# Kernel tuning notes

Measured on AMD Instinct MI355X. Metric: run time of the kernel, lower is better.

## Reference

```python
import jax, jax.numpy as jnp
import numpy as np

K = 8           # neighbor_num
H = 8           # n_heads
DH = 64         # dim_single_head


def setup_inputs() -> dict:
    key = jax.random.key(0)
    ks = jax.random.split(key, 6)
    B, N, D = 2, 8192, 256
    inner = H * DH  # 512
    x = jax.random.normal(ks[0], (B, N, D), jnp.float32)
    center_pos3d = jax.random.normal(ks[1], (B, N, 3), jnp.float32)
    Wq = jax.random.normal(ks[2], (D, inner), jnp.float32) * 0.02
    Wkv = jax.random.normal(ks[3], (D, 2 * inner), jnp.float32) * 0.02
    Wout = jax.random.normal(ks[4], (inner, D), jnp.float32) * 0.02
    bout = jnp.zeros((D,), jnp.float32)
    return {"x": x, "center_pos3d": center_pos3d, "Wq": Wq, "Wkv": Wkv,
            "Wout": Wout, "bout": bout}


def _knn_idx(pos, k):
    # pos: [B,N,3] -> indices of k nearest neighbors per point, [B,N,k]
    sq = jnp.sum(pos * pos, axis=-1)                      # [B,N]
    d2 = sq[:, :, None] + sq[:, None, :] - 2.0 * jnp.einsum('bnc,bmc->bnm', pos, pos)
    _, idx = jax.lax.top_k(-d2, k)                        # smallest distances
    return idx


def reference(x, center_pos3d, Wq, Wkv, Wout, bout):
    B, N, D = x.shape
    inner = H * DH
    scale = DH ** -0.5

    idx = _knn_idx(center_pos3d, K)                       # [B,N,K] int32
    # grouping_operation: gather neighbor features -> [B,N,K,D]
    knn_x = jax.vmap(lambda xb, ib: xb[ib])(x, idx)

    q = (x @ Wq).reshape(B, N, H, DH)                     # [B,N,H,DH]
    kv = knn_x @ Wkv                                      # [B,N,K,2*inner]
    k_, v_ = jnp.split(kv, 2, axis=-1)
    k_ = k_.reshape(B, N, K, H, DH)
    v_ = v_.reshape(B, N, K, H, DH)

    dots = jnp.einsum('bnhd,bnkhd->bnhk', q, k_) * scale  # [B,N,H,K]
    attn = jax.nn.softmax(dots, axis=-1)
    out = jnp.einsum('bnhk,bnkhd->bnhd', attn, v_)        # [B,N,H,DH]
    out = out.reshape(B, N, inner)
    return out @ Wout + bout                              # dropout p=0 -> identity
```

## Files before the change

### kernel.cpp

```cpp
#include <hip/hip_runtime.h>
#include <hip/hip_bf16.h>

#define N_PTS 8192
#define KNN 8

typedef __attribute__((ext_vector_type(8))) short short8;
typedef __attribute__((ext_vector_type(4))) float float4v;

static __device__ __forceinline__ short f2bf(float f) {
    unsigned u = __float_as_uint(f);
    unsigned r = (u + 0x7FFFu + ((u >> 16) & 1u)) >> 16;
    return (short)r;
}
static __device__ __forceinline__ float bf2f(short s) {
    return __uint_as_float(((unsigned)(unsigned short)s) << 16);
}

__global__ __launch_bounds__(256) void knn_partial(const float* __restrict__ pos,
                                                   unsigned long long* __restrict__ partial)
{
    __shared__ float sx[512], sy[512], sz[512];
    __shared__ unsigned long long buf[256][17];

    const int tid = threadIdx.x;
    const int p   = blockIdx.x & 15;
    const int qg  = blockIdx.x >> 4;
    const int batch = qg >> 5;
    const int q_in_b = (qg & 31) * 256 + tid;
    const float* bpos = pos + (long)batch * N_PTS * 3;

    if (tid < 128) {
        const float* src = bpos + (p * 512 + tid * 4) * 3;
        const float4 f0 = *(const float4*)(src);
        const float4 f1 = *(const float4*)(src + 4);
        const float4 f2 = *(const float4*)(src + 8);
        const int c0 = tid * 4;
        *(float4*)&sx[c0] = make_float4(f0.x, f0.w, f1.z, f2.y);
        *(float4*)&sy[c0] = make_float4(f0.y, f1.x, f1.w, f2.z);
        *(float4*)&sz[c0] = make_float4(f0.z, f1.y, f2.x, f2.w);
    }
    __syncthreads();

    const float qx = bpos[q_in_b * 3 + 0];
    const float qy = bpos[q_in_b * 3 + 1];
    const float qz = bpos[q_in_b * 3 + 2];

    const float4* vx = (const float4*)sx;
    const float4* vy = (const float4*)sy;
    const float4* vz = (const float4*)sz;

    float bmin[32];
#pragma unroll
    for (int j = 0; j < 32; ++j) bmin[j] = 3.0e38f;

    for (int base = 0; base < 128; base += 8) {
#pragma unroll
        for (int g = 0; g < 8; ++g) {
            const float4 cx = vx[base + g];
            const float4 cy = vy[base + g];
            const float4 cz = vz[base + g];
            { const float dx = cx.x - qx, dy = cy.x - qy, dz = cz.x - qz;
              bmin[g*4+0] = fminf(bmin[g*4+0], fmaf(dx, dx, fmaf(dy, dy, dz*dz))); }
            { const float dx = cx.y - qx, dy = cy.y - qy, dz = cz.y - qz;
              bmin[g*4+1] = fminf(bmin[g*4+1], fmaf(dx, dx, fmaf(dy, dy, dz*dz))); }
            { const float dx = cx.z - qx, dy = cy.z - qy, dz = cz.z - qz;
              bmin[g*4+2] = fminf(bmin[g*4+2], fmaf(dx, dx, fmaf(dy, dy, dz*dz))); }
            { const float dx = cx.w - qx, dy = cy.w - qy, dz = cz.w - qz;
              bmin[g*4+3] = fminf(bmin[g*4+3], fmaf(dx, dx, fmaf(dy, dy, dz*dz))); }
        }
    }

    float t8[8];
#pragma unroll
    for (int j = 0; j < 8; ++j) t8[j] = 3.0e38f;
#pragma unroll
    for (int i = 0; i < 32; ++i) {
        float x = bmin[i];
#pragma unroll
        for (int j = 0; j < 8; ++j) {
            const float lo = fminf(t8[j], x);
            const float hi = fmaxf(t8[j], x);
            t8[j] = lo; x = hi;
        }
    }
    const float t = t8[7];

    int cnt = 0;
    for (int base = 0; base < 128; ++base) {
        const float4 cx = vx[base];
        const float4 cy = vy[base];
        const float4 cz = vz[base];
#pragma unroll
        for (int j = 0; j < 4; ++j) {
            const float ccx = j == 0 ? cx.x : j == 1 ? cx.y : j == 2 ? cx.z : cx.w;
            const float ccy = j == 0 ? cy.x : j == 1 ? cy.y : j == 2 ? cy.z : cy.w;
            const float ccz = j == 0 ? cz.x : j == 1 ? cz.y : j == 2 ? cz.z : cz.w;
            const float dx = ccx - qx, dy = ccy - qy, dz = ccz - qz;
            const float d2 = fmaf(dx, dx, fmaf(dy, dy, dz * dz));
            if (d2 <= t) {
                buf[tid][cnt < 16 ? cnt : 16] =
                    ((unsigned long long)__float_as_uint(d2) << 32)
                    | (unsigned)(p * 512 + base * 4 + j);
                ++cnt;
            }
        }
    }

    unsigned long long best[8];
#pragma unroll
    for (int j = 0; j < 8; ++j) best[j] = ~0ULL;

    if (cnt <= 16) {
        for (int u = 0; u < cnt; ++u) {
            unsigned long long x = buf[tid][u];
#pragma unroll
            for (int j = 0; j < 8; ++j) {
                const unsigned long long lo = x < best[j] ? x : best[j];
                const unsigned long long hi = x < best[j] ? best[j] : x;
                best[j] = lo; x = hi;
            }
        }
    } else {
        for (int i = 0; i < 512; ++i) {
            const float dx = sx[i] - qx, dy = sy[i] - qy, dz = sz[i] - qz;
            const float d2 = fmaf(dx, dx, fmaf(dy, dy, dz * dz));
            unsigned long long x =
                ((unsigned long long)__float_as_uint(d2) << 32)
                | (unsigned)(p * 512 + i);
            if (x < best[7]) {
#pragma unroll
                for (int j = 0; j < 8; ++j) {
                    const unsigned long long lo = x < best[j] ? x : best[j];
                    const unsigned long long hi = x < best[j] ? best[j] : x;
                    best[j] = lo; x = hi;
                }
            }
        }
    }

    const long qglob = (long)batch * N_PTS + q_in_b;
#pragma unroll
    for (int j = 0; j < 8; ++j)
        partial[(long)(p * 8 + j) * 16384 + qglob] = best[j];
}

__global__ __launch_bounds__(256) void knn_merge(const unsigned long long* __restrict__ partial,
                                                 int* __restrict__ idxo)
{
    const int q = blockIdx.x * 256 + threadIdx.x;
    unsigned long long best[8];
#pragma unroll
    for (int j = 0; j < 8; ++j) best[j] = ~0ULL;
    for (int s = 0; s < 128; ++s) {
        unsigned long long x = partial[(long)s * 16384 + q];
        if (x < best[7]) {
#pragma unroll
            for (int j = 0; j < 8; ++j) {
                const unsigned long long lo = x < best[j] ? x : best[j];
                const unsigned long long hi = x < best[j] ? best[j] : x;
                best[j] = lo; x = hi;
            }
        }
    }
#pragma unroll
    for (int j = 0; j < 8; ++j)
        idxo[(long)q * 8 + j] = (int)(best[j] & 0xFFFFFFFFu);
}

template<int ABF16, int OUTBF16>
__global__ __launch_bounds__(256) void gemm_bf16(const void* __restrict__ A_,
                                                 const float* __restrict__ B,
                                                 const float* __restrict__ bias,
                                                 void* __restrict__ C_,
                                                 int N, int Kd, int lda)
{
    __shared__ short As[4][128][8];
    __shared__ short Bs[4][128][8];

    const int tid  = threadIdx.x;
    const int lane = tid & 63;
    const int wv   = tid >> 6;
    const int quad = lane >> 4;
    const int l15  = lane & 15;
    const int m0 = blockIdx.y * 128;
    const int n0 = blockIdx.x * 128;
    const int mh = (wv & 1) * 64, nh = (wv >> 1) * 64;

    const int sm  = tid >> 1;
    const int skh = (tid & 1) * 16;
    const int sn  = tid & 127;
    const int skb = (tid >> 7) * 16;

    float4v acc[4][4];
#pragma unroll
    for (int i = 0; i < 4; ++i)
#pragma unroll
        for (int j = 0; j < 4; ++j) acc[i][j] = (float4v)(0.f);

    for (int k0 = 0; k0 < Kd; k0 += 32) {
        if (ABF16) {
            const short* Ab = (const short*)A_;
            const short8* src = (const short8*)(Ab + (long)(m0 + sm) * lda + k0 + skh);
            *(short8*)&As[skh >> 3][sm][0] = src[0];
            *(short8*)&As[(skh >> 3) + 1][sm][0] = src[1];
        } else {
            const float* Af = (const float*)A_;
            const float* ap = Af + (long)(m0 + sm) * lda + k0 + skh;
            const float4 a0 = *(const float4*)ap;
            const float4 a1 = *(const float4*)(ap + 4);
            const float4 a2 = *(const float4*)(ap + 8);
            const float4 a3 = *(const float4*)(ap + 12);
            short8 w0 = {f2bf(a0.x), f2bf(a0.y), f2bf(a0.z), f2bf(a0.w),
                         f2bf(a1.x), f2bf(a1.y), f2bf(a1.z), f2bf(a1.w)};
            short8 w1 = {f2bf(a2.x), f2bf(a2.y), f2bf(a2.z), f2bf(a2.w),
                         f2bf(a3.x), f2bf(a3.y), f2bf(a3.z), f2bf(a3.w)};
            *(short8*)&As[skh >> 3][sm][0] = w0;
            *(short8*)&As[(skh >> 3) + 1][sm][0] = w1;
        }
        {
            const float* bp = B + (long)(k0 + skb) * N + n0 + sn;
            short v[16];
#pragma unroll
            for (int kk = 0; kk < 16; ++kk)
                v[kk] = f2bf(bp[(long)kk * N]);
            short8 w0 = {v[0], v[1], v[2], v[3], v[4], v[5], v[6], v[7]};
            short8 w1 = {v[8], v[9], v[10], v[11], v[12], v[13], v[14], v[15]};
            *(short8*)&Bs[skb >> 3][sn][0] = w0;
            *(short8*)&Bs[(skb >> 3) + 1][sn][0] = w1;
        }
        __syncthreads();

        short8 af[4], bfv[4];
#pragma unroll
        for (int i = 0; i < 4; ++i)
            af[i] = *(const short8*)&As[quad][mh + i * 16 + l15][0];
#pragma unroll
        for (int j = 0; j < 4; ++j)
            bfv[j] = *(const short8*)&Bs[quad][nh + j * 16 + l15][0];
#pragma unroll
        for (int i = 0; i < 4; ++i)
#pragma unroll
            for (int j = 0; j < 4; ++j)
                acc[i][j] = __builtin_amdgcn_mfma_f32_16x16x32_bf16(af[i], bfv[j], acc[i][j], 0, 0, 0);
        __syncthreads();
    }

#pragma unroll
    for (int i = 0; i < 4; ++i)
#pragma unroll
        for (int j = 0; j < 4; ++j) {
            const int col = n0 + nh + j * 16 + l15;
            const float bb = (!OUTBF16 && bias) ? bias[col] : 0.f;
#pragma unroll
            for (int r = 0; r < 4; ++r) {
                const int row = m0 + mh + i * 16 + quad * 4 + r;
                if (OUTBF16) {
                    ((short*)C_)[(long)row * N + col] = f2bf(acc[i][j][r]);
                } else {
                    ((float*)C_)[(long)row * N + col] = acc[i][j][r] + bb;
                }
            }
        }
}

__global__ __launch_bounds__(256) void attn_kernel(const short* qall,
                                                   const short* __restrict__ kvall,
                                                   const int* __restrict__ idxp,
                                                   short* outp)
{
    __shared__ float attn_s[4][8][8];
    const int wave = threadIdx.x >> 6;
    const int lane = threadIdx.x & 63;
    const int g = blockIdx.x * 4 + wave;
    const int b = g >> 13;
    const int* myidx = idxp + (long)g * 8;

    {
        const int h = lane >> 3;
        const int k = lane & 7;
        const int j = myidx[k];
        const short8* qrow = (const short8*)(qall + (long)g * 512 + h * 64);
        const short8* krow = (const short8*)(kvall + ((long)(b * N_PTS + j)) * 1024 + h * 64);

        float dot = 0.f;
#pragma unroll
        for (int c = 0; c < 8; ++c) {
            const short8 qv = qrow[c];
            const short8 kv = krow[c];
#pragma unroll
            for (int e = 0; e < 8; ++e)
                dot = fmaf(bf2f(qv[e]), bf2f(kv[e]), dot);
        }
        dot *= 0.125f;

        float m = dot;
#pragma unroll
        for (int off = 1; off < 8; off <<= 1)
            m = fmaxf(m, __shfl_xor(m, off, 8));
        const float e = __expf(dot - m);
        float ssum = e;
#pragma unroll
        for (int off = 1; off < 8; off <<= 1)
            ssum += __shfl_xor(ssum, off, 8);
        attn_s[wave][h][k] = e / ssum;
    }
    __syncthreads();

    const int d8 = lane * 8;
    const int h2 = lane >> 3;
    float o[8] = {0.f, 0.f, 0.f, 0.f, 0.f, 0.f, 0.f, 0.f};
#pragma unroll
    for (int kk = 0; kk < 8; ++kk) {
        const int jj = myidx[kk];
        const float w = attn_s[wave][h2][kk];
        const short8 v = *(const short8*)(kvall + ((long)(b * N_PTS + jj)) * 1024 + 512 + d8);
#pragma unroll
        for (int e = 0; e < 8; ++e)
            o[e] = fmaf(w, bf2f(v[e]), o[e]);
    }
    short8 ov = {f2bf(o[0]), f2bf(o[1]), f2bf(o[2]), f2bf(o[3]),
                 f2bf(o[4]), f2bf(o[5]), f2bf(o[6]), f2bf(o[7])};
    *(short8*)(outp + (long)g * 512 + d8) = ov;
}

extern "C" void kernel_launch(void* const* d_in, const int* in_sizes, int n_in,
                              void* d_out, int out_size, void* d_ws, size_t ws_size,
                              hipStream_t stream)
{
    const float* x    = (const float*)d_in[0];
    const float* pos  = (const float*)d_in[1];
    const float* Wq   = (const float*)d_in[2];
    const float* Wkv  = (const float*)d_in[3];
    const float* Wout = (const float*)d_in[4];
    const float* bout = (const float*)d_in[5];
    float* out = (float*)d_out;

    int*   idxp = (int*)d_ws;
    short* qall = (short*)((char*)d_ws + (1 << 19));
    short* kvall = qall + (long)16384 * 512;
    unsigned long long* partial = (unsigned long long*)kvall;

    const int M = 16384;

    knn_partial<<<1024, 256, 0, stream>>>(pos, partial);
    knn_merge<<<64, 256, 0, stream>>>(partial, idxp);
    gemm_bf16<0, 1><<<dim3(512 / 128, M / 128), 256, 0, stream>>>(x, Wq, nullptr, qall, 512, 256, 256);
    gemm_bf16<0, 1><<<dim3(1024 / 128, M / 128), 256, 0, stream>>>(x, Wkv, nullptr, kvall, 1024, 256, 256);
    attn_kernel<<<M / 4, 256, 0, stream>>>(qall, kvall, idxp, qall);
    gemm_bf16<1, 0><<<dim3(256 / 128, M / 128), 256, 0, stream>>>(qall, Wout, bout, out, 256, 512, 512);
}
```

Measured before the change: 321.5 us.

## Use dot-product KNN with larger tiles and pre-converted bf16 GEMM operands

The KNN partial kernel now stores each candidate as a float4 holding xyz and half its squared norm. It screens candidates with a single 3-FMA dot-product score instead of a full distance, and processes 1024 candidates per block, which halves the partial slices and the merge work. A small epsilon widens the screening threshold, and exact distances are recomputed for the final ordering. The GEMMs now read x and transposed weights that separate conversion kernels have already turned into bf16, which removes per-tile fp32-to-bf16 conversion and the strided weight loads. This adds extra kernel launches and conversion passes on every call.

```diff
diff --git a/kernel.cpp b/kernel.cpp
--- a/kernel.cpp
+++ b/kernel.cpp
@@ -6,6 +6,7 @@
 
 typedef __attribute__((ext_vector_type(8))) short short8;
 typedef __attribute__((ext_vector_type(4))) float float4v;
+typedef unsigned long long u64;
 
 static __device__ __forceinline__ short f2bf(float f) {
     unsigned u = __float_as_uint(f);
@@ -17,27 +18,31 @@
 }
 
 __global__ __launch_bounds__(256) void knn_partial(const float* __restrict__ pos,
-                                                   unsigned long long* __restrict__ partial)
-{
-    __shared__ float sx[512], sy[512], sz[512];
-    __shared__ unsigned long long buf[256][17];
+                                                   u64* __restrict__ partial)
+{
+    __shared__ float4 sc[1024];
+    __shared__ u64 buf[256][17];
 
     const int tid = threadIdx.x;
-    const int p   = blockIdx.x & 15;
-    const int qg  = blockIdx.x >> 4;
+    const int p   = blockIdx.x & 7;
+    const int qg  = blockIdx.x >> 3;
     const int batch = qg >> 5;
     const int q_in_b = (qg & 31) * 256 + tid;
     const float* bpos = pos + (long)batch * N_PTS * 3;
 
-    if (tid < 128) {
-        const float* src = bpos + (p * 512 + tid * 4) * 3;
+    {
+        const float* src = bpos + (p * 1024 + tid * 4) * 3;
         const float4 f0 = *(const float4*)(src);
         const float4 f1 = *(const float4*)(src + 4);
         const float4 f2 = *(const float4*)(src + 8);
-        const int c0 = tid * 4;
-        *(float4*)&sx[c0] = make_float4(f0.x, f0.w, f1.z, f2.y);
-        *(float4*)&sy[c0] = make_float4(f0.y, f1.x, f1.w, f2.z);
-        *(float4*)&sz[c0] = make_float4(f0.z, f1.y, f2.x, f2.w);
+        sc[tid * 4 + 0] = make_float4(f0.x, f0.y, f0.z,
+            0.5f * fmaf(f0.x, f0.x, fmaf(f0.y, f0.y, f0.z * f0.z)));
+        sc[tid * 4 + 1] = make_float4(f0.w, f1.x, f1.y,
+            0.5f * fmaf(f0.w, f0.w, fmaf(f1.x, f1.x, f1.y * f1.y)));
+        sc[tid * 4 + 2] = make_float4(f1.z, f1.w, f2.x,
+            0.5f * fmaf(f1.z, f1.z, fmaf(f1.w, f1.w, f2.x * f2.x)));
+        sc[tid * 4 + 3] = make_float4(f2.y, f2.z, f2.w,
+            0.5f * fmaf(f2.y, f2.y, fmaf(f2.z, f2.z, f2.w * f2.w)));
     }
     __syncthreads();
 
@@ -45,28 +50,16 @@
     const float qy = bpos[q_in_b * 3 + 1];
     const float qz = bpos[q_in_b * 3 + 2];
 
-    const float4* vx = (const float4*)sx;
-    const float4* vy = (const float4*)sy;
-    const float4* vz = (const float4*)sz;
-
     float bmin[32];
 #pragma unroll
     for (int j = 0; j < 32; ++j) bmin[j] = 3.0e38f;
 
-    for (int base = 0; base < 128; base += 8) {
-#pragma unroll
-        for (int g = 0; g < 8; ++g) {
-            const float4 cx = vx[base + g];
-            const float4 cy = vy[base + g];
-            const float4 cz = vz[base + g];
-            { const float dx = cx.x - qx, dy = cy.x - qy, dz = cz.x - qz;
-              bmin[g*4+0] = fminf(bmin[g*4+0], fmaf(dx, dx, fmaf(dy, dy, dz*dz))); }
-            { const float dx = cx.y - qx, dy = cy.y - qy, dz = cz.y - qz;
-              bmin[g*4+1] = fminf(bmin[g*4+1], fmaf(dx, dx, fmaf(dy, dy, dz*dz))); }
-            { const float dx = cx.z - qx, dy = cy.z - qy, dz = cz.z - qz;
-              bmin[g*4+2] = fminf(bmin[g*4+2], fmaf(dx, dx, fmaf(dy, dy, dz*dz))); }
-            { const float dx = cx.w - qx, dy = cy.w - qy, dz = cz.w - qz;
-              bmin[g*4+3] = fminf(bmin[g*4+3], fmaf(dx, dx, fmaf(dy, dy, dz*dz))); }
+    for (int base = 0; base < 1024; base += 32) {
+#pragma unroll
+        for (int j = 0; j < 32; ++j) {
+            const float4 c = sc[base + j];
+            const float s = fmaf(-qx, c.x, fmaf(-qy, c.y, fmaf(-qz, c.z, c.w)));
+            bmin[j] = fminf(bmin[j], s);
         }
     }
 
@@ -83,55 +76,46 @@
             t8[j] = lo; x = hi;
         }
     }
-    const float t = t8[7];
+    const float t = t8[7] + 1e-4f;
 
     int cnt = 0;
-    for (int base = 0; base < 128; ++base) {
-        const float4 cx = vx[base];
-        const float4 cy = vy[base];
-        const float4 cz = vz[base];
-#pragma unroll
-        for (int j = 0; j < 4; ++j) {
-            const float ccx = j == 0 ? cx.x : j == 1 ? cx.y : j == 2 ? cx.z : cx.w;
-            const float ccy = j == 0 ? cy.x : j == 1 ? cy.y : j == 2 ? cy.z : cy.w;
-            const float ccz = j == 0 ? cz.x : j == 1 ? cz.y : j == 2 ? cz.z : cz.w;
-            const float dx = ccx - qx, dy = ccy - qy, dz = ccz - qz;
+    for (int i = 0; i < 1024; ++i) {
+        const float4 c = sc[i];
+        const float s = fmaf(-qx, c.x, fmaf(-qy, c.y, fmaf(-qz, c.z, c.w)));
+        if (s <= t) {
+            const float dx = c.x - qx, dy = c.y - qy, dz = c.z - qz;
             const float d2 = fmaf(dx, dx, fmaf(dy, dy, dz * dz));
-            if (d2 <= t) {
-                buf[tid][cnt < 16 ? cnt : 16] =
-                    ((unsigned long long)__float_as_uint(d2) << 32)
-                    | (unsigned)(p * 512 + base * 4 + j);
-                ++cnt;
-            }
-        }
-    }
-
-    unsigned long long best[8];
+            buf[tid][cnt < 16 ? cnt : 16] =
+                ((u64)__float_as_uint(d2) << 32) | (unsigned)(p * 1024 + i);
+            ++cnt;
+        }
+    }
+
+    u64 best[8];
 #pragma unroll
     for (int j = 0; j < 8; ++j) best[j] = ~0ULL;
 
     if (cnt <= 16) {
         for (int u = 0; u < cnt; ++u) {
-            unsigned long long x = buf[tid][u];
+            u64 x = buf[tid][u];
 #pragma unroll
             for (int j = 0; j < 8; ++j) {
-                const unsigned long long lo = x < best[j] ? x : best[j];
-                const unsigned long long hi = x < best[j] ? best[j] : x;
+                const u64 lo = x < best[j] ? x : best[j];
+                const u64 hi = x < best[j] ? best[j] : x;
                 best[j] = lo; x = hi;
             }
         }
     } else {
-        for (int i = 0; i < 512; ++i) {
-            const float dx = sx[i] - qx, dy = sy[i] - qy, dz = sz[i] - qz;
+        for (int i = 0; i < 1024; ++i) {
+            const float4 c = sc[i];
+            const float dx = c.x - qx, dy = c.y - qy, dz = c.z - qz;
             const float d2 = fmaf(dx, dx, fmaf(dy, dy, dz * dz));
-            unsigned long long x =
-                ((unsigned long long)__float_as_uint(d2) << 32)
-                | (unsigned)(p * 512 + i);
+            u64 x = ((u64)__float_as_uint(d2) << 32) | (unsigned)(p * 1024 + i);
             if (x < best[7]) {
 #pragma unroll
                 for (int j = 0; j < 8; ++j) {
-                    const unsigned long long lo = x < best[j] ? x : best[j];
-                    const unsigned long long hi = x < best[j] ? best[j] : x;
+                    const u64 lo = x < best[j] ? x : best[j];
+                    const u64 hi = x < best[j] ? best[j] : x;
                     best[j] = lo; x = hi;
                 }
             }
@@ -144,20 +128,20 @@
         partial[(long)(p * 8 + j) * 16384 + qglob] = best[j];
 }
 
-__global__ __launch_bounds__(256) void knn_merge(const unsigned long long* __restrict__ partial,
+__global__ __launch_bounds__(256) void knn_merge(const u64* __restrict__ partial,
                                                  int* __restrict__ idxo)
 {
     const int q = blockIdx.x * 256 + threadIdx.x;
-    unsigned long long best[8];
+    u64 best[8];
 #pragma unroll
     for (int j = 0; j < 8; ++j) best[j] = ~0ULL;
-    for (int s = 0; s < 128; ++s) {
-        unsigned long long x = partial[(long)s * 16384 + q];
+    for (int s = 0; s < 64; ++s) {
+        u64 x = partial[(long)s * 16384 + q];
         if (x < best[7]) {
 #pragma unroll
             for (int j = 0; j < 8; ++j) {
-                const unsigned long long lo = x < best[j] ? x : best[j];
-                const unsigned long long hi = x < best[j] ? best[j] : x;
+                const u64 lo = x < best[j] ? x : best[j];
+                const u64 hi = x < best[j] ? best[j] : x;
                 best[j] = lo; x = hi;
             }
         }
@@ -167,15 +151,37 @@
         idxo[(long)q * 8 + j] = (int)(best[j] & 0xFFFFFFFFu);
 }
 
-template<int ABF16, int OUTBF16>
-__global__ __launch_bounds__(256) void gemm_bf16(const void* __restrict__ A_,
-                                                 const float* __restrict__ B,
-                                                 const float* __restrict__ bias,
-                                                 void* __restrict__ C_,
-                                                 int N, int Kd, int lda)
-{
-    __shared__ short As[4][128][8];
-    __shared__ short Bs[4][128][8];
+__global__ __launch_bounds__(256) void conv_x(const float* __restrict__ x,
+                                              short* __restrict__ xb)
+{
+    const int i = blockIdx.x * 256 + threadIdx.x;
+    const float4 a = ((const float4*)x)[i * 2];
+    const float4 b = ((const float4*)x)[i * 2 + 1];
+    short8 w = {f2bf(a.x), f2bf(a.y), f2bf(a.z), f2bf(a.w),
+                f2bf(b.x), f2bf(b.y), f2bf(b.z), f2bf(b.w)};
+    ((short8*)xb)[i] = w;
+}
+
+__global__ __launch_bounds__(256) void conv_wt(const float* __restrict__ W,
+                                               short* __restrict__ Wt,
+                                               int kshift, int N)
+{
+    const int o = blockIdx.x * 256 + threadIdx.x;
+    const int K = 1 << kshift;
+    const int n = o >> kshift;
+    const int k = o & (K - 1);
+    Wt[o] = f2bf(W[(long)k * N + n]);
+}
+
+template<int OUTBF16>
+__global__ __launch_bounds__(256) void gemm_tt(const short* __restrict__ A,
+                                               const short* __restrict__ Bt,
+                                               const float* __restrict__ bias,
+                                               void* __restrict__ C_,
+                                               int N, int Kd)
+{
+    __shared__ short As[128][40];
+    __shared__ short Bs[128][40];
 
     const int tid  = threadIdx.x;
     const int lane = tid & 63;
@@ -186,10 +192,8 @@
     const int n0 = blockIdx.x * 128;
     const int mh = (wv & 1) * 64, nh = (wv >> 1) * 64;
 
-    const int sm  = tid >> 1;
-    const int skh = (tid & 1) * 16;
-    const int sn  = tid & 127;
-    const int skb = (tid >> 7) * 16;
+    const int srow  = tid >> 1;
+    const int shalf = (tid & 1) * 16;
 
     float4v acc[4][4];
 #pragma unroll
@@ -198,45 +202,21 @@
         for (int j = 0; j < 4; ++j) acc[i][j] = (float4v)(0.f);
 
     for (int k0 = 0; k0 < Kd; k0 += 32) {
-        if (ABF16) {
-            const short* Ab = (const short*)A_;
-            const short8* src = (const short8*)(Ab + (long)(m0 + sm) * lda + k0 + skh);
-            *(short8*)&As[skh >> 3][sm][0] = src[0];
-            *(short8*)&As[(skh >> 3) + 1][sm][0] = src[1];
-        } else {
-            const float* Af = (const float*)A_;
-            const float* ap = Af + (long)(m0 + sm) * lda + k0 + skh;
-            const float4 a0 = *(const float4*)ap;
-            const float4 a1 = *(const float4*)(ap + 4);
-            const float4 a2 = *(const float4*)(ap + 8);
-            const float4 a3 = *(const float4*)(ap + 12);
-            short8 w0 = {f2bf(a0.x), f2bf(a0.y), f2bf(a0.z), f2bf(a0.w),
-                         f2bf(a1.x), f2bf(a1.y), f2bf(a1.z), f2bf(a1.w)};
-            short8 w1 = {f2bf(a2.x), f2bf(a2.y), f2bf(a2.z), f2bf(a2.w),
-                         f2bf(a3.x), f2bf(a3.y), f2bf(a3.z), f2bf(a3.w)};
-            *(short8*)&As[skh >> 3][sm][0] = w0;
-            *(short8*)&As[(skh >> 3) + 1][sm][0] = w1;
-        }
-        {
-            const float* bp = B + (long)(k0 + skb) * N + n0 + sn;
-            short v[16];
-#pragma unroll
-            for (int kk = 0; kk < 16; ++kk)
-                v[kk] = f2bf(bp[(long)kk * N]);
-            short8 w0 = {v[0], v[1], v[2], v[3], v[4], v[5], v[6], v[7]};
-            short8 w1 = {v[8], v[9], v[10], v[11], v[12], v[13], v[14], v[15]};
-            *(short8*)&Bs[skb >> 3][sn][0] = w0;
-            *(short8*)&Bs[(skb >> 3) + 1][sn][0] = w1;
-        }
+        const short8* asrc = (const short8*)(A + (long)(m0 + srow) * Kd + k0 + shalf);
+        const short8* bsrc = (const short8*)(Bt + (long)(n0 + srow) * Kd + k0 + shalf);
+        *(short8*)&As[srow][shalf]     = asrc[0];
+        *(short8*)&As[srow][shalf + 8] = asrc[1];
+        *(short8*)&Bs[srow][shalf]     = bsrc[0];
+        *(short8*)&Bs[srow][shalf + 8] = bsrc[1];
         __syncthreads();
 
         short8 af[4], bfv[4];
 #pragma unroll
         for (int i = 0; i < 4; ++i)
-            af[i] = *(const short8*)&As[quad][mh + i * 16 + l15][0];
+            af[i] = *(const short8*)&As[mh + i * 16 + l15][quad * 8];
 #pragma unroll
         for (int j = 0; j < 4; ++j)
-            bfv[j] = *(const short8*)&Bs[quad][nh + j * 16 + l15][0];
+            bfv[j] = *(const short8*)&Bs[nh + j * 16 + l15][quad * 8];
 #pragma unroll
         for (int i = 0; i < 4; ++i)
 #pragma unroll
@@ -335,17 +315,28 @@
     const float* bout = (const float*)d_in[5];
     float* out = (float*)d_out;
 
-    int*   idxp = (int*)d_ws;
-    short* qall = (short*)((char*)d_ws + (1 << 19));
-    short* kvall = qall + (long)16384 * 512;
-    unsigned long long* partial = (unsigned long long*)kvall;
-
     const int M = 16384;
 
-    knn_partial<<<1024, 256, 0, stream>>>(pos, partial);
+    char* ws = (char*)d_ws;
+    int*   idxp  = (int*)ws;                          ws += 1 << 19;
+    short* qall  = (short*)ws;                        ws += (long)M * 512 * 2;
+    short* kvall = (short*)ws;                        ws += (long)M * 1024 * 2;
+    short* xb    = (short*)ws;                        ws += (long)M * 256 * 2;
+    short* wqt   = (short*)ws;                        ws += 512 * 256 * 2;
+    short* wkvt  = (short*)ws;                        ws += 1024 * 256 * 2;
+    short* woutt = (short*)ws;                        ws += 256 * 512 * 2;
+    u64* partial = (u64*)kvall;
+
+    knn_partial<<<512, 256, 0, stream>>>(pos, partial);
     knn_merge<<<64, 256, 0, stream>>>(partial, idxp);
-    gemm_bf16<0, 1><<<dim3(512 / 128, M / 128), 256, 0, stream>>>(x, Wq, nullptr, qall, 512, 256, 256);
-    gemm_bf16<0, 1><<<dim3(1024 / 128, M / 128), 256, 0, stream>>>(x, Wkv, nullptr, kvall, 1024, 256, 256);
+
+    conv_x<<<2048, 256, 0, stream>>>(x, xb);
+    conv_wt<<<512, 256, 0, stream>>>(Wq, wqt, 8, 512);
+    conv_wt<<<1024, 256, 0, stream>>>(Wkv, wkvt, 8, 1024);
+    conv_wt<<<512, 256, 0, stream>>>(Wout, woutt, 9, 256);
+
+    gemm_tt<1><<<dim3(4, 128), 256, 0, stream>>>(xb, wqt, nullptr, qall, 512, 256);
+    gemm_tt<1><<<dim3(8, 128), 256, 0, stream>>>(xb, wkvt, nullptr, kvall, 1024, 256);
     attn_kernel<<<M / 4, 256, 0, stream>>>(qall, kvall, idxp, qall);
-    gemm_bf16<1, 0><<<dim3(256 / 128, M / 128), 256, 0, stream>>>(qall, Wout, bout, out, 256, 512, 512);
-}
+    gemm_tt<0><<<dim3(2, 128), 256, 0, stream>>>(qall, woutt, bout, out, 256, 512);
+}
```

Result: slower. 410.2 us (+27.6%).
